# Kernel tuning notes

Hardware: AMD Instinct MI355X
Metric: run time of the kernel (lower is better)

Reference implementation:

```python
import jax, jax.numpy as jnp
import numpy as np
from jax import lax

B, T, D = 16384, 60, 36   # n_traj, n_tp, n_dims
L, C, S = 10, 20, 9       # latent_dim, cluster_num, n_static
OUT = 8                   # mlp out (use_static=False)


def setup_inputs() -> dict:
    key = jax.random.key(0)
    ks = jax.random.split(key, 12)

    def w(k, shape):
        return jax.random.normal(k, shape, jnp.float32) / np.float32(np.sqrt(shape[0]))

    return {
        "data": jax.random.normal(ks[0], (B, T, D), jnp.float32),
        "time_steps": jnp.arange(T, dtype=jnp.float32),
        "static_data": jax.random.normal(ks[1], (B, S), jnp.float32),
        # GRU_unit_cluster gates: Linear(latent_dim + input_dim -> latent_dim)
        "W_update": w(ks[2], (L + D, L)), "b_update": jnp.zeros((L,), jnp.float32),
        "W_reset": w(ks[3], (L + D, L)), "b_reset": jnp.zeros((L,), jnp.float32),
        "W_new": w(ks[4], (L + D, L)), "b_new": jnp.zeros((L,), jnp.float32),
        # infer_emitter_z: Linear(latent_dim + cluster_num -> cluster_num)
        "W_emit": w(ks[5], (L + C, C)), "b_emit": jnp.zeros((C,), jnp.float32),
        # stand-in ODE func (z0_diffeq_solver.ode_func): tanh(Linear(latent->latent))
        "W_ode": w(ks[6], (L, L)), "b_ode": jnp.zeros((L,), jnp.float32),
        # final mlp: Linear(ts*10 + static -> 8)
        "W_mlp": w(ks[7], (T * L + S, OUT)), "b_mlp": jnp.zeros((OUT,), jnp.float32),
    }


def _forward(data, time_steps, static_data,
             W_update, b_update, W_reset, b_reset, W_new, b_new,
             W_emit, b_emit, W_ode, b_ode, W_mlp, b_mlp):
    n_traj = data.shape[0]
    # per-step dt: first step uses the synthetic 0.01 offset, then consecutive diffs
    dts = jnp.concatenate([jnp.full((1,), 0.01, time_steps.dtype), jnp.diff(time_steps)])
    xs = jnp.swapaxes(data, 0, 1)  # [T, B, D]

    def step(carry, inp):
        y_state, y_prob = carry        # [B, L], [B, C]
        x_t, dt = inp                  # [B, D], scalar
        # Euler step of the ODE between observations
        yi_ode = y_state + jnp.tanh(y_state @ W_ode + b_ode) * dt
        # GRU_unit_cluster update
        yc = jnp.concatenate([yi_ode, x_t], axis=-1)          # [B, L+D]
        u = jax.nn.sigmoid(yc @ W_update + b_update)
        r = jax.nn.sigmoid(yc @ W_reset + b_reset)
        cc = jnp.concatenate([yi_ode * r, x_t], axis=-1)
        new = cc @ W_new + b_new
        y_new = (1.0 - u) * new + u * yi_ode                  # [B, L]
        # emit_probs (concat_data=True path)
        zin = jnp.concatenate([y_prob, y_new], axis=-1)       # [B, C+L]
        y_prob_new = jax.nn.softmax(zin @ W_emit + b_emit, axis=-1)
        return (y_new, y_prob_new), y_new

    init = (jnp.zeros((n_traj, L), data.dtype), jnp.zeros((n_traj, C), data.dtype))
    _, states = lax.scan(step, init, (xs, dts))               # states: [T, B, L]

    vec = jnp.swapaxes(states, 0, 1).reshape(n_traj, T * L)   # [B, T*L]
    vec = jnp.concatenate([vec, static_data], axis=-1)        # [B, T*L + S]
    return vec @ W_mlp + b_mlp                                # [B, 8]


def reference(data, time_steps, static_data,
              W_update, b_update, W_reset, b_reset, W_new, b_new,
              W_emit, b_emit, W_ode, b_ode, W_mlp, b_mlp):
    return _forward(data, time_steps, static_data,
                    W_update, b_update, W_reset, b_reset, W_new, b_new,
                    W_emit, b_emit, W_ode, b_ode, W_mlp, b_mlp)
```

## Files before the change

### kernel.cpp

```cpp
#include <hip/hip_runtime.h>
#include <hip/hip_fp16.h>
#include <math.h>

#define B_TRAJ 16384
#define T_STEPS 60
#define D_IN 36
#define L_DIM 10
#define C_NUM 20
#define S_STAT 9
#define OUT_DIM 8
#define TT 2
#define NTILE (T_STEPS / TT)
#define XTS 1824

#define LOG2E 1.4426950408889634f

typedef float f32x2 __attribute__((ext_vector_type(2)));
__device__ __forceinline__ f32x2 pkfma(f32x2 a, f32x2 b, f32x2 c) {
    return __builtin_elementwise_fma(a, b, c);
}

__device__ __forceinline__ float rcp_fast(float x) { return __builtin_amdgcn_rcpf(x); }
__device__ __forceinline__ float exp2_fast(float x) { return __builtin_amdgcn_exp2f(x); }
__device__ __forceinline__ float sigm_fast(float x) {
    return rcp_fast(1.0f + exp2_fast(x * -LOG2E));
}
__device__ __forceinline__ float tanh_fast(float x) {
    const float t = fminf(fmaxf(x * (2.0f * LOG2E), -30.0f), 30.0f);
    return fmaf(-2.0f, rcp_fast(exp2_fast(t) + 1.0f), 1.0f);
}
#define WFENCE() __builtin_amdgcn_wave_barrier()

__global__ __launch_bounds__(256) __attribute__((amdgpu_waves_per_eu(4, 8)))
void dgm2_v8(
    const float* __restrict__ data,
    const float* __restrict__ time_steps,
    const float* __restrict__ static_data,
    const float* __restrict__ W_update,
    const float* __restrict__ b_update,
    const float* __restrict__ W_reset,
    const float* __restrict__ b_reset,
    const float* __restrict__ W_new,
    const float* __restrict__ b_new,
    const float* __restrict__ W_emit,
    const float* __restrict__ b_emit,
    const float* __restrict__ W_ode,
    const float* __restrict__ b_ode,
    const float* __restrict__ W_mlp,
    const float* __restrict__ b_mlp,
    float* __restrict__ out)
{
    __shared__ __align__(16) __half xprojH[8 * XTS];
    __shared__ __align__(16) float wbuf[4][144];
    __shared__ float dts[T_STEPS];

    const int tid  = threadIdx.x;
    const int w    = tid >> 6;
    const int lane = tid & 63;
    const int half = lane >> 5;
    const int s    = lane & 31;
    const int ltraj = w * 2 + half;
    const int traj  = blockIdx.x * 8 + ltraj;
    __half* xpj = xprojH + ltraj * XTS;

    if (tid < T_STEPS) dts[tid] = (tid == 0) ? 0.01f : time_steps[tid] - time_steps[tid - 1];
    __syncthreads();

    const bool uo = (s < 10);
    const bool ro = (s >= 10 && s < 20);
    const bool no = (s >= 20 && s < 30);
    const bool eo = (s >= 10 && s < 30);
    const int  gcol = uo ? s : (ro ? (s - 10) : (no ? (s - 20) : 0));
    const float* Wg = uo ? W_update : (ro ? W_reset : W_new);

    float bcol = 0.0f;
    if (uo)      bcol = b_update[s];
    else if (ro) bcol = b_reset[s - 10];
    else if (no) bcol = b_new[s - 20];

    {
        f32x2 wxp2[18];
#pragma unroll
        for (int j = 0; j < 18; ++j)
            wxp2[j] = (f32x2){Wg[(L_DIM + 2 * j) * L_DIM + gcol],
                              Wg[(L_DIM + 2 * j + 1) * L_DIM + gcol]};

        float* xst = &wbuf[w][0];
        const float* tbase = data + (size_t)(blockIdx.x * 8 + w * 2) * (T_STEPS * D_IN);
        const int sh  = lane / 18;
        const int sr  = lane % 18;
        const int stt = sr / 9;
        const int sc  = sr % 9;
        const bool stg = (lane < 36);

        if (stg) {
            const float4 v = *reinterpret_cast<const float4*>(
                tbase + (size_t)sh * (T_STEPS * D_IN) + stt * D_IN + sc * 4);
            *reinterpret_cast<float4*>(xst + (sh * TT + stt) * 36 + sc * 4) = v;
        }
        WFENCE();

        for (int tile = 0; tile < NTILE; ++tile) {
            float4 pf = make_float4(0.f, 0.f, 0.f, 0.f);
            const bool more = stg && (tile + 1 < NTILE);
            if (more) {
                pf = *reinterpret_cast<const float4*>(
                    tbase + (size_t)sh * (T_STEPS * D_IN) + ((tile + 1) * TT + stt) * D_IN + sc * 4);
            }
#pragma unroll
            for (int tt = 0; tt < TT; ++tt) {
                const float* xrow = xst + (half * TT + tt) * 36;
                f32x2 acc2 = (f32x2){bcol, 0.0f};
#pragma unroll
                for (int c = 0; c < 9; ++c) {
                    const float4 x4 = *reinterpret_cast<const float4*>(xrow + c * 4);
                    acc2 = pkfma((f32x2){x4.x, x4.y}, wxp2[2 * c],     acc2);
                    acc2 = pkfma((f32x2){x4.z, x4.w}, wxp2[2 * c + 1], acc2);
                }
                if (s < 30) xpj[(tile * TT + tt) * 30 + s] = __float2half(acc2.x + acc2.y);
            }
            WFENCE();
            if (more) {
                *reinterpret_cast<float4*>(xst + (sh * TT + stt) * 36 + sc * 4) = pf;
            }
            WFENCE();
        }
    }

    f32x2 wgy2[5];
#pragma unroll
    for (int j = 0; j < 5; ++j)
        wgy2[j] = (f32x2){Wg[(2 * j) * L_DIM + gcol], Wg[(2 * j + 1) * L_DIM + gcol]};

    f32x2 waux2[15];
#pragma unroll
    for (int j = 0; j < 15; ++j) {
        float v0 = 0.0f, v1 = 0.0f;
        if (eo)               { v0 = W_emit[(2 * j) * C_NUM + (s - 10)];
                                v1 = W_emit[(2 * j + 1) * C_NUM + (s - 10)]; }
        else if (uo && j < 5) { v0 = W_ode[(2 * j) * L_DIM + s];
                                v1 = W_ode[(2 * j + 1) * L_DIM + s]; }
        waux2[j] = (f32x2){v0, v1};
    }
    const float bode  = uo ? b_ode[s] : 0.0f;
    const float bemit = eo ? b_emit[s - 10] : 0.0f;

    float* wb   = &wbuf[w][0];
    float* bcYI = wb + 0  + half * 12;
    float* bcR  = wb + 24 + half * 12;
    float* bcU  = wb + 48 + half * 12;
    float* bcY  = wb + 72 + half * 12;
    float* bcP  = wb + 96 + half * 20;

    f32x2 y2[5];
#pragma unroll
    for (int k = 0; k < 5; ++k) y2[k] = (f32x2){0.0f, 0.0f};
    float yown = 0.0f;
    if (eo) bcP[s - 10] = 0.0f;
    WFENCE();

    for (int t = 0; t < T_STEPS; ++t) {
        const float dt = dts[t];

        f32x2 g2 = (f32x2){bode, 0.0f};
#pragma unroll
        for (int k = 0; k < 5; ++k) g2 = pkfma(y2[k], waux2[k], g2);
        const float yis = fmaf(tanh_fast(g2.x + g2.y), dt, yown);
        if (uo) bcYI[s] = yis;
        WFENCE();
        {
            const float4 a = *reinterpret_cast<const float4*>(bcYI);
            const float4 b = *reinterpret_cast<const float4*>(bcYI + 4);
            const float2 c = *reinterpret_cast<const float2*>(bcYI + 8);
            y2[0] = (f32x2){a.x, a.y}; y2[1] = (f32x2){a.z, a.w};
            y2[2] = (f32x2){b.x, b.y}; y2[3] = (f32x2){b.z, b.w};
            y2[4] = (f32x2){c.x, c.y};
        }
        const float yi_g = bcYI[gcol];

        const float xa = __half2float(xpj[t * 30 + s]);
        f32x2 ay2 = (f32x2){xa, 0.0f};
#pragma unroll
        for (int k = 0; k < 5; ++k) ay2 = pkfma(y2[k], wgy2[k], ay2);
        const float uval = sigm_fast(ay2.x + ay2.y);
        if (ro) bcR[s - 10] = uval * yi_g;
        if (uo) bcU[s] = uval;
        WFENCE();

        f32x2 n2 = (f32x2){xa, 0.0f};
        {
            const float4 a = *reinterpret_cast<const float4*>(bcR);
            const float4 b = *reinterpret_cast<const float4*>(bcR + 4);
            const float2 c = *reinterpret_cast<const float2*>(bcR + 8);
            n2 = pkfma((f32x2){a.x, a.y}, wgy2[0], n2);
            n2 = pkfma((f32x2){a.z, a.w}, wgy2[1], n2);
            n2 = pkfma((f32x2){b.x, b.y}, wgy2[2], n2);
            n2 = pkfma((f32x2){b.z, b.w}, wgy2[3], n2);
            n2 = pkfma((f32x2){c.x, c.y}, wgy2[4], n2);
        }
        const float accN = n2.x + n2.y;
        const float u_n  = bcU[gcol];
        const float yn   = fmaf(u_n, yi_g - accN, accN);
        if (no) {
            bcY[s - 20] = yn;
            xpj[t * 30 + (s - 20)] = __float2half(yn);
        }
        WFENCE();
        {
            const float4 a = *reinterpret_cast<const float4*>(bcY);
            const float4 b = *reinterpret_cast<const float4*>(bcY + 4);
            const float2 c = *reinterpret_cast<const float2*>(bcY + 8);
            y2[0] = (f32x2){a.x, a.y}; y2[1] = (f32x2){a.z, a.w};
            y2[2] = (f32x2){b.x, b.y}; y2[3] = (f32x2){b.z, b.w};
            y2[4] = (f32x2){c.x, c.y};
        }
        yown = bcY[gcol];

        f32x2 zd2 = (f32x2){0.0f, 0.0f};
        f32x2 zs2 = (f32x2){0.0f, 0.0f};
#pragma unroll
        for (int q = 0; q < 5; ++q) {
            const float4 z4 = *reinterpret_cast<const float4*>(bcP + q * 4);
            const f32x2 za = (f32x2){z4.x, z4.y};
            const f32x2 zb = (f32x2){z4.z, z4.w};
            zd2 = pkfma(za, waux2[2 * q],     zd2);
            zd2 = pkfma(zb, waux2[2 * q + 1], zd2);
            zs2 = zs2 + za + zb;
        }
        const float zsum = zs2.x + zs2.y;
        const float pinv = (t == 0) ? 0.0f : rcp_fast(zsum);
        f32x2 ev2 = (f32x2){fmaf(zd2.x + zd2.y, pinv, bemit), 0.0f};
#pragma unroll
        for (int k = 0; k < 5; ++k) ev2 = pkfma(y2[k], waux2[10 + k], ev2);
        const float zv = exp2_fast(fminf((ev2.x + ev2.y) * LOG2E, 86.0f));
        if (eo) bcP[s - 10] = zv;
    }

    WFENCE();
    {
        const int g = s >> 3, col = s & 7;
        f32x2 o2 = (f32x2){0.0f, 0.0f};
        for (int tb = 0; tb < 15; ++tb) {
            const int t = g + tb * 4;
            const __half2* yh = reinterpret_cast<const __half2*>(xpj + t * 30);
            const float* wrow = W_mlp + (size_t)t * L_DIM * OUT_DIM + col;
#pragma unroll
            for (int q = 0; q < 5; ++q) {
                const float2 yv = __half22float2(yh[q]);
                const f32x2 w2 = (f32x2){wrow[(2 * q) * OUT_DIM], wrow[(2 * q + 1) * OUT_DIM]};
                o2 = pkfma((f32x2){yv.x, yv.y}, w2, o2);
            }
        }
        float o8 = o2.x + o2.y;
        o8 += __shfl_xor(o8, 8, 32);
        o8 += __shfl_xor(o8, 16, 32);
        if (s < OUT_DIM) {
            const float* stp = static_data + (size_t)traj * S_STAT;
            const float* wms = W_mlp + (size_t)(T_STEPS * L_DIM) * OUT_DIM;
#pragma unroll
            for (int i = 0; i < S_STAT; ++i) o8 += stp[i] * wms[i * OUT_DIM + s];
            out[(size_t)traj * OUT_DIM + s] = o8 + b_mlp[s];
        }
    }
}

extern "C" void kernel_launch(void* const* d_in, const int* in_sizes, int n_in,
                              void* d_out, int out_size, void* d_ws, size_t ws_size,
                              hipStream_t stream) {
    const float* data        = (const float*)d_in[0];
    const float* time_steps  = (const float*)d_in[1];
    const float* static_data = (const float*)d_in[2];
    const float* W_update    = (const float*)d_in[3];
    const float* b_update    = (const float*)d_in[4];
    const float* W_reset     = (const float*)d_in[5];
    const float* b_reset     = (const float*)d_in[6];
    const float* W_new       = (const float*)d_in[7];
    const float* b_new       = (const float*)d_in[8];
    const float* W_emit      = (const float*)d_in[9];
    const float* b_emit      = (const float*)d_in[10];
    const float* W_ode       = (const float*)d_in[11];
    const float* b_ode       = (const float*)d_in[12];
    const float* W_mlp       = (const float*)d_in[13];
    const float* b_mlp       = (const float*)d_in[14];
    float* out = (float*)d_out;

    dim3 grid(B_TRAJ / 8), block(256);
    hipLaunchKernelGGL(dgm2_v8, grid, block, 0, stream,
                       data, time_steps, static_data,
                       W_update, b_update, W_reset, b_reset, W_new, b_new,
                       W_emit, b_emit, W_ode, b_ode, W_mlp, b_mlp, out);
}
```

Measured before the change: 330.6 us.

## Remap recurrence to 16 lanes per trajectory with single-wave blocks

Each trajectory now gets 16 lanes instead of 32. Every lane computes its own update, reset and new gate column, plus up to two emitter columns. The recurrent step drops from four wave-local exchanges to three because the u value no longer needs to be broadcast. Blocks shrink to one wave with four trajectories each, so each wave does twice the useful work and barriers are cheaper. In exchange each lane holds more registers for weights, which may lower occupancy, and the serial dependency chain per lane gets longer.

```diff
diff --git a/kernel.cpp b/kernel.cpp
--- a/kernel.cpp
+++ b/kernel.cpp
@@ -12,6 +12,7 @@
 #define TT 2
 #define NTILE (T_STEPS / TT)
 #define XTS 1824
+#define GSTRIDE 88
 
 #define LOG2E 1.4426950408889634f
 
@@ -19,7 +20,6 @@
 __device__ __forceinline__ f32x2 pkfma(f32x2 a, f32x2 b, f32x2 c) {
     return __builtin_elementwise_fma(a, b, c);
 }
-
 __device__ __forceinline__ float rcp_fast(float x) { return __builtin_amdgcn_rcpf(x); }
 __device__ __forceinline__ float exp2_fast(float x) { return __builtin_amdgcn_exp2f(x); }
 __device__ __forceinline__ float sigm_fast(float x) {
@@ -31,8 +31,8 @@
 }
 #define WFENCE() __builtin_amdgcn_wave_barrier()
 
-__global__ __launch_bounds__(256) __attribute__((amdgpu_waves_per_eu(4, 8)))
-void dgm2_v8(
+__global__ __launch_bounds__(64)
+void dgm2_v9(
     const float* __restrict__ data,
     const float* __restrict__ time_steps,
     const float* __restrict__ static_data,
@@ -50,113 +50,159 @@
     const float* __restrict__ b_mlp,
     float* __restrict__ out)
 {
-    __shared__ __align__(16) __half xprojH[8 * XTS];
-    __shared__ __align__(16) float wbuf[4][144];
+    __shared__ __align__(16) __half xprojH[4 * XTS];
+    __shared__ __align__(16) float wbuf[4 * GSTRIDE];
     __shared__ float dts[T_STEPS];
 
     const int tid  = threadIdx.x;
-    const int w    = tid >> 6;
-    const int lane = tid & 63;
-    const int half = lane >> 5;
-    const int s    = lane & 31;
-    const int ltraj = w * 2 + half;
-    const int traj  = blockIdx.x * 8 + ltraj;
-    __half* xpj = xprojH + ltraj * XTS;
+    const int g    = tid >> 4;
+    const int q    = tid & 15;
+    const int traj = blockIdx.x * 4 + g;
+    __half* xpj = xprojH + g * XTS;
 
     if (tid < T_STEPS) dts[tid] = (tid == 0) ? 0.01f : time_steps[tid] - time_steps[tid - 1];
-    __syncthreads();
-
-    const bool uo = (s < 10);
-    const bool ro = (s >= 10 && s < 20);
-    const bool no = (s >= 20 && s < 30);
-    const bool eo = (s >= 10 && s < 30);
-    const int  gcol = uo ? s : (ro ? (s - 10) : (no ? (s - 20) : 0));
-    const float* Wg = uo ? W_update : (ro ? W_reset : W_new);
-
-    float bcol = 0.0f;
-    if (uo)      bcol = b_update[s];
-    else if (ro) bcol = b_reset[s - 10];
-    else if (no) bcol = b_new[s - 20];
+    WFENCE();
+
+    auto gate_ptr = [&](int c) -> const float* {
+        return c < 10 ? W_update : (c < 20 ? W_reset : W_new);
+    };
+    auto gate_col = [&](int c) -> int { return c < 10 ? c : (c < 20 ? c - 10 : c - 20); };
+    auto gate_bias = [&](int c) -> float {
+        return c < 10 ? b_update[c] : (c < 20 ? b_reset[c - 10] : b_new[c - 20]);
+    };
 
     {
-        f32x2 wxp2[18];
-#pragma unroll
-        for (int j = 0; j < 18; ++j)
-            wxp2[j] = (f32x2){Wg[(L_DIM + 2 * j) * L_DIM + gcol],
-                              Wg[(L_DIM + 2 * j + 1) * L_DIM + gcol]};
-
-        float* xst = &wbuf[w][0];
-        const float* tbase = data + (size_t)(blockIdx.x * 8 + w * 2) * (T_STEPS * D_IN);
-        const int sh  = lane / 18;
-        const int sr  = lane % 18;
-        const int stt = sr / 9;
-        const int sc  = sr % 9;
-        const bool stg = (lane < 36);
-
-        if (stg) {
-            const float4 v = *reinterpret_cast<const float4*>(
-                tbase + (size_t)sh * (T_STEPS * D_IN) + stt * D_IN + sc * 4);
-            *reinterpret_cast<float4*>(xst + (sh * TT + stt) * 36 + sc * 4) = v;
+        const int  c0   = q;
+        const bool has1 = (q < 14);
+        const int  c1   = has1 ? 16 + q : 29;
+        const float* W0 = gate_ptr(c0); const int cc0 = gate_col(c0);
+        const float* W1 = gate_ptr(c1); const int cc1 = gate_col(c1);
+
+        f32x2 wxp0[18], wxp1[18];
+#pragma unroll
+        for (int j = 0; j < 18; ++j) {
+            wxp0[j] = (f32x2){W0[(L_DIM + 2 * j) * L_DIM + cc0],
+                              W0[(L_DIM + 2 * j + 1) * L_DIM + cc0]};
+            const f32x2 v1 = (f32x2){W1[(L_DIM + 2 * j) * L_DIM + cc1],
+                                     W1[(L_DIM + 2 * j + 1) * L_DIM + cc1]};
+            wxp1[j] = has1 ? v1 : (f32x2){0.0f, 0.0f};
+        }
+        const float bcol0 = gate_bias(c0);
+        const float bcol1 = has1 ? gate_bias(c1) : 0.0f;
+
+        float* stagef = wbuf;
+        const float* tb0 = data + (size_t)(blockIdx.x * 4) * (T_STEPS * D_IN);
+        const int a_tr = tid / 18, a_rm = tid % 18, a_tt = a_rm / 9, a_c = a_rm % 9;
+        const int bch = 64 + tid;
+        const int b_tr = bch / 18, b_rm = bch % 18, b_tt = b_rm / 9, b_c = b_rm % 9;
+        const bool hb = (tid < 8);
+
+        {
+            const float4 v0 = *reinterpret_cast<const float4*>(
+                tb0 + (size_t)a_tr * (T_STEPS * D_IN) + a_tt * D_IN + a_c * 4);
+            *reinterpret_cast<float4*>(stagef + (a_tr * TT + a_tt) * 36 + a_c * 4) = v0;
+            if (hb) {
+                const float4 v1 = *reinterpret_cast<const float4*>(
+                    tb0 + (size_t)b_tr * (T_STEPS * D_IN) + b_tt * D_IN + b_c * 4);
+                *reinterpret_cast<float4*>(stagef + (b_tr * TT + b_tt) * 36 + b_c * 4) = v1;
+            }
         }
         WFENCE();
 
         for (int tile = 0; tile < NTILE; ++tile) {
-            float4 pf = make_float4(0.f, 0.f, 0.f, 0.f);
-            const bool more = stg && (tile + 1 < NTILE);
+            float4 pf0 = {}, pf1 = {};
+            const bool more = (tile + 1 < NTILE);
             if (more) {
-                pf = *reinterpret_cast<const float4*>(
-                    tbase + (size_t)sh * (T_STEPS * D_IN) + ((tile + 1) * TT + stt) * D_IN + sc * 4);
+                pf0 = *reinterpret_cast<const float4*>(
+                    tb0 + (size_t)a_tr * (T_STEPS * D_IN) + ((tile + 1) * TT + a_tt) * D_IN + a_c * 4);
+                if (hb)
+                    pf1 = *reinterpret_cast<const float4*>(
+                        tb0 + (size_t)b_tr * (T_STEPS * D_IN) + ((tile + 1) * TT + b_tt) * D_IN + b_c * 4);
             }
 #pragma unroll
             for (int tt = 0; tt < TT; ++tt) {
-                const float* xrow = xst + (half * TT + tt) * 36;
-                f32x2 acc2 = (f32x2){bcol, 0.0f};
+                const float* xrow = stagef + (g * TT + tt) * 36;
+                f32x2 acc0 = (f32x2){bcol0, 0.0f};
+                f32x2 acc1 = (f32x2){bcol1, 0.0f};
 #pragma unroll
                 for (int c = 0; c < 9; ++c) {
                     const float4 x4 = *reinterpret_cast<const float4*>(xrow + c * 4);
-                    acc2 = pkfma((f32x2){x4.x, x4.y}, wxp2[2 * c],     acc2);
-                    acc2 = pkfma((f32x2){x4.z, x4.w}, wxp2[2 * c + 1], acc2);
+                    const f32x2 xlo = (f32x2){x4.x, x4.y};
+                    const f32x2 xhi = (f32x2){x4.z, x4.w};
+                    acc0 = pkfma(xlo, wxp0[2 * c], acc0);
+                    acc0 = pkfma(xhi, wxp0[2 * c + 1], acc0);
+                    acc1 = pkfma(xlo, wxp1[2 * c], acc1);
+                    acc1 = pkfma(xhi, wxp1[2 * c + 1], acc1);
                 }
-                if (s < 30) xpj[(tile * TT + tt) * 30 + s] = __float2half(acc2.x + acc2.y);
+                const int row = (tile * TT + tt) * 30;
+                xpj[row + q] = __float2half(acc0.x + acc0.y);
+                if (has1) xpj[row + 16 + q] = __float2half(acc1.x + acc1.y);
             }
             WFENCE();
             if (more) {
-                *reinterpret_cast<float4*>(xst + (sh * TT + stt) * 36 + sc * 4) = pf;
+                *reinterpret_cast<float4*>(stagef + (a_tr * TT + a_tt) * 36 + a_c * 4) = pf0;
+                if (hb)
+                    *reinterpret_cast<float4*>(stagef + (b_tr * TT + b_tt) * 36 + b_c * 4) = pf1;
             }
             WFENCE();
         }
     }
 
-    f32x2 wgy2[5];
-#pragma unroll
-    for (int j = 0; j < 5; ++j)
-        wgy2[j] = (f32x2){Wg[(2 * j) * L_DIM + gcol], Wg[(2 * j + 1) * L_DIM + gcol]};
-
-    f32x2 waux2[15];
-#pragma unroll
-    for (int j = 0; j < 15; ++j) {
-        float v0 = 0.0f, v1 = 0.0f;
-        if (eo)               { v0 = W_emit[(2 * j) * C_NUM + (s - 10)];
-                                v1 = W_emit[(2 * j + 1) * C_NUM + (s - 10)]; }
-        else if (uo && j < 5) { v0 = W_ode[(2 * j) * L_DIM + s];
-                                v1 = W_ode[(2 * j + 1) * L_DIM + s]; }
-        waux2[j] = (f32x2){v0, v1};
-    }
-    const float bode  = uo ? b_ode[s] : 0.0f;
-    const float bemit = eo ? b_emit[s - 10] : 0.0f;
-
-    float* wb   = &wbuf[w][0];
-    float* bcYI = wb + 0  + half * 12;
-    float* bcR  = wb + 24 + half * 12;
-    float* bcU  = wb + 48 + half * 12;
-    float* bcY  = wb + 72 + half * 12;
-    float* bcP  = wb + 96 + half * 20;
+    const bool qg = (q < 10);
+    f32x2 wode2[5], wu2[5], wr2[5], wn2[5];
+#pragma unroll
+    for (int j = 0; j < 5; ++j) {
+        if (qg) {
+            wode2[j] = (f32x2){W_ode[(2 * j) * L_DIM + q], W_ode[(2 * j + 1) * L_DIM + q]};
+            wu2[j]   = (f32x2){W_update[(2 * j) * L_DIM + q], W_update[(2 * j + 1) * L_DIM + q]};
+            wr2[j]   = (f32x2){W_reset[(2 * j) * L_DIM + q], W_reset[(2 * j + 1) * L_DIM + q]};
+            wn2[j]   = (f32x2){W_new[(2 * j) * L_DIM + q], W_new[(2 * j + 1) * L_DIM + q]};
+        } else {
+            wode2[j] = wu2[j] = wr2[j] = wn2[j] = (f32x2){0.0f, 0.0f};
+        }
+    }
+    const float bode = qg ? b_ode[q] : 0.0f;
+
+    const int  e0  = q;
+    const bool he1 = (q < 4);
+    const int  e1  = he1 ? 16 + q : 19;
+    f32x2 wez0[10], wez1[10], wey0[5], wey1[5];
+#pragma unroll
+    for (int j = 0; j < 10; ++j) {
+        wez0[j] = (f32x2){W_emit[(2 * j) * C_NUM + e0], W_emit[(2 * j + 1) * C_NUM + e0]};
+        const f32x2 v1 = (f32x2){W_emit[(2 * j) * C_NUM + e1], W_emit[(2 * j + 1) * C_NUM + e1]};
+        wez1[j] = he1 ? v1 : (f32x2){0.0f, 0.0f};
+    }
+#pragma unroll
+    for (int j = 0; j < 5; ++j) {
+        wey0[j] = (f32x2){W_emit[(C_NUM + 2 * j) * C_NUM + e0], W_emit[(C_NUM + 2 * j + 1) * C_NUM + e0]};
+        const f32x2 v1 = (f32x2){W_emit[(C_NUM + 2 * j) * C_NUM + e1], W_emit[(C_NUM + 2 * j + 1) * C_NUM + e1]};
+        wey1[j] = he1 ? v1 : (f32x2){0.0f, 0.0f};
+    }
+    const float be0 = b_emit[e0];
+    const float be1 = he1 ? b_emit[e1] : 0.0f;
+
+    float* grp = wbuf + g * GSTRIDE;
+    float* gYI = grp;
+    float* gYR = grp + 16;
+    float* gY  = grp + 32;
+    float* gZ  = grp + 48;
+
+    auto ldvec = [&](const float* p, f32x2* d) {
+        const float4 a = *reinterpret_cast<const float4*>(p);
+        const float4 b = *reinterpret_cast<const float4*>(p + 4);
+        const float2 c = *reinterpret_cast<const float2*>(p + 8);
+        d[0] = (f32x2){a.x, a.y}; d[1] = (f32x2){a.z, a.w};
+        d[2] = (f32x2){b.x, b.y}; d[3] = (f32x2){b.z, b.w};
+        d[4] = (f32x2){c.x, c.y};
+    };
 
     f32x2 y2[5];
 #pragma unroll
     for (int k = 0; k < 5; ++k) y2[k] = (f32x2){0.0f, 0.0f};
     float yown = 0.0f;
-    if (eo) bcP[s - 10] = 0.0f;
+    gZ[q] = 0.0f;
+    if (he1) gZ[16 + q] = 0.0f;
     WFENCE();
 
     for (int t = 0; t < T_STEPS; ++t) {
@@ -164,102 +210,100 @@
 
         f32x2 g2 = (f32x2){bode, 0.0f};
 #pragma unroll
-        for (int k = 0; k < 5; ++k) g2 = pkfma(y2[k], waux2[k], g2);
+        for (int k = 0; k < 5; ++k) g2 = pkfma(y2[k], wode2[k], g2);
         const float yis = fmaf(tanh_fast(g2.x + g2.y), dt, yown);
-        if (uo) bcYI[s] = yis;
+        gYI[q] = yis;
         WFENCE();
+        f32x2 yi2[5];
+        ldvec(gYI, yi2);
+
+        const float xau = __half2float(xpj[t * 30 + q]);
+        const float xar = __half2float(xpj[t * 30 + 10 + q]);
+        const float xan = __half2float(xpj[t * 30 + 20 + q]);
+        f32x2 au2 = (f32x2){xau, 0.0f};
+        f32x2 ar2 = (f32x2){xar, 0.0f};
+#pragma unroll
+        for (int k = 0; k < 5; ++k) {
+            au2 = pkfma(yi2[k], wu2[k], au2);
+            ar2 = pkfma(yi2[k], wr2[k], ar2);
+        }
+        const float u = sigm_fast(au2.x + au2.y);
+        const float r = sigm_fast(ar2.x + ar2.y);
+        gYR[q] = r * yis;
+        WFENCE();
+        f32x2 yr2[5];
+        ldvec(gYR, yr2);
+
+        f32x2 an2 = (f32x2){xan, 0.0f};
+#pragma unroll
+        for (int k = 0; k < 5; ++k) an2 = pkfma(yr2[k], wn2[k], an2);
+        const float nv = an2.x + an2.y;
+        const float yn = fmaf(u, yis - nv, nv);
+        yown = yn;
+        gY[q] = yn;
+        xpj[t * 30 + q] = __float2half(yn);
+        WFENCE();
+        ldvec(gY, y2);
+
+        f32x2 zz[10];
         {
-            const float4 a = *reinterpret_cast<const float4*>(bcYI);
-            const float4 b = *reinterpret_cast<const float4*>(bcYI + 4);
-            const float2 c = *reinterpret_cast<const float2*>(bcYI + 8);
-            y2[0] = (f32x2){a.x, a.y}; y2[1] = (f32x2){a.z, a.w};
-            y2[2] = (f32x2){b.x, b.y}; y2[3] = (f32x2){b.z, b.w};
-            y2[4] = (f32x2){c.x, c.y};
-        }
-        const float yi_g = bcYI[gcol];
-
-        const float xa = __half2float(xpj[t * 30 + s]);
-        f32x2 ay2 = (f32x2){xa, 0.0f};
-#pragma unroll
-        for (int k = 0; k < 5; ++k) ay2 = pkfma(y2[k], wgy2[k], ay2);
-        const float uval = sigm_fast(ay2.x + ay2.y);
-        if (ro) bcR[s - 10] = uval * yi_g;
-        if (uo) bcU[s] = uval;
-        WFENCE();
-
-        f32x2 n2 = (f32x2){xa, 0.0f};
-        {
-            const float4 a = *reinterpret_cast<const float4*>(bcR);
-            const float4 b = *reinterpret_cast<const float4*>(bcR + 4);
-            const float2 c = *reinterpret_cast<const float2*>(bcR + 8);
-            n2 = pkfma((f32x2){a.x, a.y}, wgy2[0], n2);
-            n2 = pkfma((f32x2){a.z, a.w}, wgy2[1], n2);
-            n2 = pkfma((f32x2){b.x, b.y}, wgy2[2], n2);
-            n2 = pkfma((f32x2){b.z, b.w}, wgy2[3], n2);
-            n2 = pkfma((f32x2){c.x, c.y}, wgy2[4], n2);
-        }
-        const float accN = n2.x + n2.y;
-        const float u_n  = bcU[gcol];
-        const float yn   = fmaf(u_n, yi_g - accN, accN);
-        if (no) {
-            bcY[s - 20] = yn;
-            xpj[t * 30 + (s - 20)] = __float2half(yn);
-        }
-        WFENCE();
-        {
-            const float4 a = *reinterpret_cast<const float4*>(bcY);
-            const float4 b = *reinterpret_cast<const float4*>(bcY + 4);
-            const float2 c = *reinterpret_cast<const float2*>(bcY + 8);
-            y2[0] = (f32x2){a.x, a.y}; y2[1] = (f32x2){a.z, a.w};
-            y2[2] = (f32x2){b.x, b.y}; y2[3] = (f32x2){b.z, b.w};
-            y2[4] = (f32x2){c.x, c.y};
-        }
-        yown = bcY[gcol];
-
-        f32x2 zd2 = (f32x2){0.0f, 0.0f};
+            const float4 z0 = *reinterpret_cast<const float4*>(gZ);
+            const float4 z1 = *reinterpret_cast<const float4*>(gZ + 4);
+            const float4 z2 = *reinterpret_cast<const float4*>(gZ + 8);
+            const float4 z3 = *reinterpret_cast<const float4*>(gZ + 12);
+            const float4 z4 = *reinterpret_cast<const float4*>(gZ + 16);
+            zz[0] = (f32x2){z0.x, z0.y}; zz[1] = (f32x2){z0.z, z0.w};
+            zz[2] = (f32x2){z1.x, z1.y}; zz[3] = (f32x2){z1.z, z1.w};
+            zz[4] = (f32x2){z2.x, z2.y}; zz[5] = (f32x2){z2.z, z2.w};
+            zz[6] = (f32x2){z3.x, z3.y}; zz[7] = (f32x2){z3.z, z3.w};
+            zz[8] = (f32x2){z4.x, z4.y}; zz[9] = (f32x2){z4.z, z4.w};
+        }
+        f32x2 zd0 = (f32x2){0.0f, 0.0f}, zd1 = (f32x2){0.0f, 0.0f};
         f32x2 zs2 = (f32x2){0.0f, 0.0f};
 #pragma unroll
-        for (int q = 0; q < 5; ++q) {
-            const float4 z4 = *reinterpret_cast<const float4*>(bcP + q * 4);
-            const f32x2 za = (f32x2){z4.x, z4.y};
-            const f32x2 zb = (f32x2){z4.z, z4.w};
-            zd2 = pkfma(za, waux2[2 * q],     zd2);
-            zd2 = pkfma(zb, waux2[2 * q + 1], zd2);
-            zs2 = zs2 + za + zb;
+        for (int j = 0; j < 10; ++j) {
+            zd0 = pkfma(zz[j], wez0[j], zd0);
+            zd1 = pkfma(zz[j], wez1[j], zd1);
+            zs2 = zs2 + zz[j];
         }
         const float zsum = zs2.x + zs2.y;
         const float pinv = (t == 0) ? 0.0f : rcp_fast(zsum);
-        f32x2 ev2 = (f32x2){fmaf(zd2.x + zd2.y, pinv, bemit), 0.0f};
-#pragma unroll
-        for (int k = 0; k < 5; ++k) ev2 = pkfma(y2[k], waux2[10 + k], ev2);
-        const float zv = exp2_fast(fminf((ev2.x + ev2.y) * LOG2E, 86.0f));
-        if (eo) bcP[s - 10] = zv;
+        f32x2 ev0 = (f32x2){fmaf(zd0.x + zd0.y, pinv, be0), 0.0f};
+        f32x2 ev1 = (f32x2){fmaf(zd1.x + zd1.y, pinv, be1), 0.0f};
+#pragma unroll
+        for (int k = 0; k < 5; ++k) {
+            ev0 = pkfma(y2[k], wey0[k], ev0);
+            ev1 = pkfma(y2[k], wey1[k], ev1);
+        }
+        const float zv0 = exp2_fast(fminf((ev0.x + ev0.y) * LOG2E, 86.0f));
+        const float zv1 = exp2_fast(fminf((ev1.x + ev1.y) * LOG2E, 86.0f));
+        gZ[q] = zv0;
+        if (he1) gZ[16 + q] = zv1;
     }
 
     WFENCE();
     {
-        const int g = s >> 3, col = s & 7;
+        const int col = q & 7, tg = q >> 3;
         f32x2 o2 = (f32x2){0.0f, 0.0f};
-        for (int tb = 0; tb < 15; ++tb) {
-            const int t = g + tb * 4;
+        for (int tb = 0; tb < 30; ++tb) {
+            const int t = tb * 2 + tg;
             const __half2* yh = reinterpret_cast<const __half2*>(xpj + t * 30);
             const float* wrow = W_mlp + (size_t)t * L_DIM * OUT_DIM + col;
 #pragma unroll
-            for (int q = 0; q < 5; ++q) {
-                const float2 yv = __half22float2(yh[q]);
-                const f32x2 w2 = (f32x2){wrow[(2 * q) * OUT_DIM], wrow[(2 * q + 1) * OUT_DIM]};
+            for (int q4 = 0; q4 < 5; ++q4) {
+                const float2 yv = __half22float2(yh[q4]);
+                const f32x2 w2 = (f32x2){wrow[(2 * q4) * OUT_DIM], wrow[(2 * q4 + 1) * OUT_DIM]};
                 o2 = pkfma((f32x2){yv.x, yv.y}, w2, o2);
             }
         }
         float o8 = o2.x + o2.y;
-        o8 += __shfl_xor(o8, 8, 32);
-        o8 += __shfl_xor(o8, 16, 32);
-        if (s < OUT_DIM) {
+        o8 += __shfl_xor(o8, 8, 16);
+        if (q < OUT_DIM) {
             const float* stp = static_data + (size_t)traj * S_STAT;
             const float* wms = W_mlp + (size_t)(T_STEPS * L_DIM) * OUT_DIM;
 #pragma unroll
-            for (int i = 0; i < S_STAT; ++i) o8 += stp[i] * wms[i * OUT_DIM + s];
-            out[(size_t)traj * OUT_DIM + s] = o8 + b_mlp[s];
+            for (int i = 0; i < S_STAT; ++i) o8 += stp[i] * wms[i * OUT_DIM + q];
+            out[(size_t)traj * OUT_DIM + q] = o8 + b_mlp[q];
         }
     }
 }
@@ -284,8 +328,8 @@
     const float* b_mlp       = (const float*)d_in[14];
     float* out = (float*)d_out;
 
-    dim3 grid(B_TRAJ / 8), block(256);
-    hipLaunchKernelGGL(dgm2_v8, grid, block, 0, stream,
+    dim3 grid(B_TRAJ / 4), block(64);
+    hipLaunchKernelGGL(dgm2_v9, grid, block, 0, stream,
                        data, time_steps, static_data,
                        W_update, b_update, W_reset, b_reset, W_new, b_new,
                        W_emit, b_emit, W_ode, b_ode, W_mlp, b_mlp, out);
```

Result: no change. 332.3 us (+0.5%).

## Chunk input projection into two halves and fuse MLP head into recurrence

Applied to the files above, without the earlier changes.

Splits the precomputed half-precision input projection into two 30-step chunks, so each trajectory needs half the LDS buffer, and halves the block to 128 threads with a higher waves-per-EU hint. The final MLP head is now accumulated step by step inside the recurrence instead of storing states and doing a separate pass afterwards. This cuts LDS footprint to raise occupancy. In exchange it pays for a mid-sequence refill that reloads the projection weights and stalls the serial recurrence, and adds global W_mlp loads on every step.

```diff
diff --git a/kernel.cpp b/kernel.cpp
--- a/kernel.cpp
+++ b/kernel.cpp
@@ -10,8 +10,10 @@
 #define S_STAT 9
 #define OUT_DIM 8
 #define TT 2
-#define NTILE (T_STEPS / TT)
-#define XTS 1824
+#define CHT 30
+#define NTILE_C (CHT / TT)
+#define XTS2 928
+#define WBF 184
 
 #define LOG2E 1.4426950408889634f
 
@@ -19,7 +21,6 @@
 __device__ __forceinline__ f32x2 pkfma(f32x2 a, f32x2 b, f32x2 c) {
     return __builtin_elementwise_fma(a, b, c);
 }
-
 __device__ __forceinline__ float rcp_fast(float x) { return __builtin_amdgcn_rcpf(x); }
 __device__ __forceinline__ float exp2_fast(float x) { return __builtin_amdgcn_exp2f(x); }
 __device__ __forceinline__ float sigm_fast(float x) {
@@ -31,8 +32,8 @@
 }
 #define WFENCE() __builtin_amdgcn_wave_barrier()
 
-__global__ __launch_bounds__(256) __attribute__((amdgpu_waves_per_eu(4, 8)))
-void dgm2_v8(
+__global__ __launch_bounds__(128) __attribute__((amdgpu_waves_per_eu(6, 8)))
+void dgm2_v14(
     const float* __restrict__ data,
     const float* __restrict__ time_steps,
     const float* __restrict__ static_data,
@@ -50,8 +51,8 @@
     const float* __restrict__ b_mlp,
     float* __restrict__ out)
 {
-    __shared__ __align__(16) __half xprojH[8 * XTS];
-    __shared__ __align__(16) float wbuf[4][144];
+    __shared__ __align__(16) __half xprojH[4 * XTS2];
+    __shared__ __align__(16) float wbuf[2][WBF];
     __shared__ float dts[T_STEPS];
 
     const int tid  = threadIdx.x;
@@ -60,8 +61,8 @@
     const int half = lane >> 5;
     const int s    = lane & 31;
     const int ltraj = w * 2 + half;
-    const int traj  = blockIdx.x * 8 + ltraj;
-    __half* xpj = xprojH + ltraj * XTS;
+    const int traj  = blockIdx.x * 4 + ltraj;
+    __half* xpj = xprojH + ltraj * XTS2;
 
     if (tid < T_STEPS) dts[tid] = (tid == 0) ? 0.01f : time_steps[tid] - time_steps[tid - 1];
     __syncthreads();
@@ -72,60 +73,6 @@
     const bool eo = (s >= 10 && s < 30);
     const int  gcol = uo ? s : (ro ? (s - 10) : (no ? (s - 20) : 0));
     const float* Wg = uo ? W_update : (ro ? W_reset : W_new);
-
-    float bcol = 0.0f;
-    if (uo)      bcol = b_update[s];
-    else if (ro) bcol = b_reset[s - 10];
-    else if (no) bcol = b_new[s - 20];
-
-    {
-        f32x2 wxp2[18];
-#pragma unroll
-        for (int j = 0; j < 18; ++j)
-            wxp2[j] = (f32x2){Wg[(L_DIM + 2 * j) * L_DIM + gcol],
-                              Wg[(L_DIM + 2 * j + 1) * L_DIM + gcol]};
-
-        float* xst = &wbuf[w][0];
-        const float* tbase = data + (size_t)(blockIdx.x * 8 + w * 2) * (T_STEPS * D_IN);
-        const int sh  = lane / 18;
-        const int sr  = lane % 18;
-        const int stt = sr / 9;
-        const int sc  = sr % 9;
-        const bool stg = (lane < 36);
-
-        if (stg) {
-            const float4 v = *reinterpret_cast<const float4*>(
-                tbase + (size_t)sh * (T_STEPS * D_IN) + stt * D_IN + sc * 4);
-            *reinterpret_cast<float4*>(xst + (sh * TT + stt) * 36 + sc * 4) = v;
-        }
-        WFENCE();
-
-        for (int tile = 0; tile < NTILE; ++tile) {
-            float4 pf = make_float4(0.f, 0.f, 0.f, 0.f);
-            const bool more = stg && (tile + 1 < NTILE);
-            if (more) {
-                pf = *reinterpret_cast<const float4*>(
-                    tbase + (size_t)sh * (T_STEPS * D_IN) + ((tile + 1) * TT + stt) * D_IN + sc * 4);
-            }
-#pragma unroll
-            for (int tt = 0; tt < TT; ++tt) {
-                const float* xrow = xst + (half * TT + tt) * 36;
-                f32x2 acc2 = (f32x2){bcol, 0.0f};
-#pragma unroll
-                for (int c = 0; c < 9; ++c) {
-                    const float4 x4 = *reinterpret_cast<const float4*>(xrow + c * 4);
-                    acc2 = pkfma((f32x2){x4.x, x4.y}, wxp2[2 * c],     acc2);
-                    acc2 = pkfma((f32x2){x4.z, x4.w}, wxp2[2 * c + 1], acc2);
-                }
-                if (s < 30) xpj[(tile * TT + tt) * 30 + s] = __float2half(acc2.x + acc2.y);
-            }
-            WFENCE();
-            if (more) {
-                *reinterpret_cast<float4*>(xst + (sh * TT + stt) * 36 + sc * 4) = pf;
-            }
-            WFENCE();
-        }
-    }
 
     f32x2 wgy2[5];
 #pragma unroll
@@ -145,12 +92,86 @@
     const float bode  = uo ? b_ode[s] : 0.0f;
     const float bemit = eo ? b_emit[s - 10] : 0.0f;
 
+    const int hcol = s & 7;
+    const int kq   = s >> 3;
+    const int boff = 2 * kq * OUT_DIM + hcol;
+    const int hoff = 2 * kq;
+    float phead = 0.0f;
+
     float* wb   = &wbuf[w][0];
-    float* bcYI = wb + 0  + half * 12;
-    float* bcR  = wb + 24 + half * 12;
-    float* bcU  = wb + 48 + half * 12;
-    float* bcY  = wb + 72 + half * 12;
-    float* bcP  = wb + 96 + half * 20;
+    float* bcYI = wb + 0   + half * 12;
+    float* bcR  = wb + 24  + half * 12;
+    float* bcU  = wb + 48  + half * 12;
+    float* bcY  = wb + 72  + half * 12;
+    float* bcP  = wb + 144 + half * 20;
+
+    auto ldvec = [&](const float* p, f32x2* d) {
+        const float4 a = *reinterpret_cast<const float4*>(p);
+        const float4 b = *reinterpret_cast<const float4*>(p + 4);
+        const float2 c = *reinterpret_cast<const float2*>(p + 8);
+        d[0] = (f32x2){a.x, a.y}; d[1] = (f32x2){a.z, a.w};
+        d[2] = (f32x2){b.x, b.y}; d[3] = (f32x2){b.z, b.w};
+        d[4] = (f32x2){c.x, c.y};
+    };
+
+    auto refill = [&](int c) {
+        asm volatile("" ::: "memory");
+        int off = 0;
+        asm volatile("" : "+v"(off));
+        f32x2 wxp2[18];
+#pragma unroll
+        for (int j = 0; j < 18; ++j)
+            wxp2[j] = (f32x2){Wg[(L_DIM + 2 * j) * L_DIM + gcol + off],
+                              Wg[(L_DIM + 2 * j + 1) * L_DIM + gcol + off]};
+        float bcol = 0.0f;
+        if (uo)      bcol = b_update[s];
+        else if (ro) bcol = b_reset[s - 10];
+        else if (no) bcol = b_new[s - 20];
+
+        float* xst = wb;
+        const float* tbase = data + (size_t)(blockIdx.x * 4 + w * 2) * (T_STEPS * D_IN);
+        const int sh  = lane / 18;
+        const int sr  = lane % 18;
+        const int stt = sr / 9;
+        const int scq = sr % 9;
+        const bool stg = (lane < 36);
+        const int cbase = c * CHT;
+
+        if (stg) {
+            const float4 v = *reinterpret_cast<const float4*>(
+                tbase + (size_t)sh * (T_STEPS * D_IN) + (cbase + stt) * D_IN + scq * 4);
+            *reinterpret_cast<float4*>(xst + (sh * TT + stt) * 36 + scq * 4) = v;
+        }
+        WFENCE();
+
+#pragma unroll 1
+        for (int tile = 0; tile < NTILE_C; ++tile) {
+            float4 pf = make_float4(0.f, 0.f, 0.f, 0.f);
+            const bool more = stg && (tile + 1 < NTILE_C);
+            if (more) {
+                pf = *reinterpret_cast<const float4*>(
+                    tbase + (size_t)sh * (T_STEPS * D_IN)
+                          + (cbase + (tile + 1) * TT + stt) * D_IN + scq * 4);
+            }
+#pragma unroll
+            for (int tt = 0; tt < TT; ++tt) {
+                const float* xrow = xst + (half * TT + tt) * 36;
+                f32x2 acc2 = (f32x2){bcol, 0.0f};
+#pragma unroll
+                for (int cq = 0; cq < 9; ++cq) {
+                    const float4 x4 = *reinterpret_cast<const float4*>(xrow + cq * 4);
+                    acc2 = pkfma((f32x2){x4.x, x4.y}, wxp2[2 * cq],     acc2);
+                    acc2 = pkfma((f32x2){x4.z, x4.w}, wxp2[2 * cq + 1], acc2);
+                }
+                if (s < 30) xpj[(tile * TT + tt) * 30 + s] = __float2half(acc2.x + acc2.y);
+            }
+            WFENCE();
+            if (more) {
+                *reinterpret_cast<float4*>(xst + (sh * TT + stt) * 36 + scq * 4) = pf;
+            }
+            WFENCE();
+        }
+    };
 
     f32x2 y2[5];
 #pragma unroll
@@ -159,108 +180,94 @@
     if (eo) bcP[s - 10] = 0.0f;
     WFENCE();
 
-    for (int t = 0; t < T_STEPS; ++t) {
-        const float dt = dts[t];
-
-        f32x2 g2 = (f32x2){bode, 0.0f};
-#pragma unroll
-        for (int k = 0; k < 5; ++k) g2 = pkfma(y2[k], waux2[k], g2);
-        const float yis = fmaf(tanh_fast(g2.x + g2.y), dt, yown);
-        if (uo) bcYI[s] = yis;
-        WFENCE();
-        {
-            const float4 a = *reinterpret_cast<const float4*>(bcYI);
-            const float4 b = *reinterpret_cast<const float4*>(bcYI + 4);
-            const float2 c = *reinterpret_cast<const float2*>(bcYI + 8);
-            y2[0] = (f32x2){a.x, a.y}; y2[1] = (f32x2){a.z, a.w};
-            y2[2] = (f32x2){b.x, b.y}; y2[3] = (f32x2){b.z, b.w};
-            y2[4] = (f32x2){c.x, c.y};
-        }
-        const float yi_g = bcYI[gcol];
-
-        const float xa = __half2float(xpj[t * 30 + s]);
-        f32x2 ay2 = (f32x2){xa, 0.0f};
-#pragma unroll
-        for (int k = 0; k < 5; ++k) ay2 = pkfma(y2[k], wgy2[k], ay2);
-        const float uval = sigm_fast(ay2.x + ay2.y);
-        if (ro) bcR[s - 10] = uval * yi_g;
-        if (uo) bcU[s] = uval;
-        WFENCE();
-
-        f32x2 n2 = (f32x2){xa, 0.0f};
-        {
-            const float4 a = *reinterpret_cast<const float4*>(bcR);
-            const float4 b = *reinterpret_cast<const float4*>(bcR + 4);
-            const float2 c = *reinterpret_cast<const float2*>(bcR + 8);
-            n2 = pkfma((f32x2){a.x, a.y}, wgy2[0], n2);
-            n2 = pkfma((f32x2){a.z, a.w}, wgy2[1], n2);
-            n2 = pkfma((f32x2){b.x, b.y}, wgy2[2], n2);
-            n2 = pkfma((f32x2){b.z, b.w}, wgy2[3], n2);
-            n2 = pkfma((f32x2){c.x, c.y}, wgy2[4], n2);
-        }
-        const float accN = n2.x + n2.y;
-        const float u_n  = bcU[gcol];
-        const float yn   = fmaf(u_n, yi_g - accN, accN);
-        if (no) {
-            bcY[s - 20] = yn;
-            xpj[t * 30 + (s - 20)] = __float2half(yn);
-        }
-        WFENCE();
-        {
-            const float4 a = *reinterpret_cast<const float4*>(bcY);
-            const float4 b = *reinterpret_cast<const float4*>(bcY + 4);
-            const float2 c = *reinterpret_cast<const float2*>(bcY + 8);
-            y2[0] = (f32x2){a.x, a.y}; y2[1] = (f32x2){a.z, a.w};
-            y2[2] = (f32x2){b.x, b.y}; y2[3] = (f32x2){b.z, b.w};
-            y2[4] = (f32x2){c.x, c.y};
-        }
-        yown = bcY[gcol];
-
-        f32x2 zd2 = (f32x2){0.0f, 0.0f};
-        f32x2 zs2 = (f32x2){0.0f, 0.0f};
-#pragma unroll
-        for (int q = 0; q < 5; ++q) {
-            const float4 z4 = *reinterpret_cast<const float4*>(bcP + q * 4);
-            const f32x2 za = (f32x2){z4.x, z4.y};
-            const f32x2 zb = (f32x2){z4.z, z4.w};
-            zd2 = pkfma(za, waux2[2 * q],     zd2);
-            zd2 = pkfma(zb, waux2[2 * q + 1], zd2);
-            zs2 = zs2 + za + zb;
-        }
-        const float zsum = zs2.x + zs2.y;
-        const float pinv = (t == 0) ? 0.0f : rcp_fast(zsum);
-        f32x2 ev2 = (f32x2){fmaf(zd2.x + zd2.y, pinv, bemit), 0.0f};
-#pragma unroll
-        for (int k = 0; k < 5; ++k) ev2 = pkfma(y2[k], waux2[10 + k], ev2);
-        const float zv = exp2_fast(fminf((ev2.x + ev2.y) * LOG2E, 86.0f));
-        if (eo) bcP[s - 10] = zv;
+    refill(0);
+    WFENCE();
+
+#pragma unroll 1
+    for (int c = 0; c < 2; ++c) {
+#pragma unroll 1
+        for (int tt = 0; tt < CHT; ++tt) {
+            const int t = c * CHT + tt;
+            const float dt = dts[t];
+
+            f32x2 g2 = (f32x2){bode, 0.0f};
+#pragma unroll
+            for (int k = 0; k < 5; ++k) g2 = pkfma(y2[k], waux2[k], g2);
+            const float yis = fmaf(tanh_fast(g2.x + g2.y), dt, yown);
+            if (uo) bcYI[s] = yis;
+            WFENCE();
+            f32x2 yi2[5];
+            ldvec(bcYI, yi2);
+            const float yi_g = bcYI[gcol];
+
+            const float xa = __half2float(xpj[tt * 30 + s]);
+            f32x2 ay2 = (f32x2){xa, 0.0f};
+#pragma unroll
+            for (int k = 0; k < 5; ++k) ay2 = pkfma(yi2[k], wgy2[k], ay2);
+            const float uval = sigm_fast(ay2.x + ay2.y);
+            if (ro) bcR[s - 10] = uval * yi_g;
+            if (uo) bcU[s] = uval;
+            WFENCE();
+            f32x2 yr2[5];
+            ldvec(bcR, yr2);
+
+            f32x2 n2 = (f32x2){xa, 0.0f};
+#pragma unroll
+            for (int k = 0; k < 5; ++k) n2 = pkfma(yr2[k], wgy2[k], n2);
+            const float accN = n2.x + n2.y;
+            const float u_n  = bcU[gcol];
+            const float yn   = fmaf(u_n, yi_g - accN, accN);
+            if (no) bcY[s - 20] = yn;
+            WFENCE();
+            ldvec(bcY, y2);
+            yown = bcY[gcol];
+
+            {
+                const float* wr = W_mlp + (size_t)t * (L_DIM * OUT_DIM);
+                const f32x2 yh = *reinterpret_cast<const f32x2*>(bcY + hoff);
+                phead = fmaf(yh.x, wr[boff], phead);
+                phead = fmaf(yh.y, wr[boff + OUT_DIM], phead);
+                if (kq == 0) {
+                    phead = fmaf(y2[4].x, wr[8 * OUT_DIM + hcol], phead);
+                    phead = fmaf(y2[4].y, wr[9 * OUT_DIM + hcol], phead);
+                }
+            }
+
+            f32x2 zz[10];
+#pragma unroll
+            for (int j = 0; j < 5; ++j) {
+                const float4 z = *reinterpret_cast<const float4*>(bcP + j * 4);
+                zz[2 * j] = (f32x2){z.x, z.y}; zz[2 * j + 1] = (f32x2){z.z, z.w};
+            }
+            f32x2 zd2 = (f32x2){0.0f, 0.0f};
+            f32x2 zs2 = (f32x2){0.0f, 0.0f};
+#pragma unroll
+            for (int j = 0; j < 10; ++j) {
+                zd2 = pkfma(zz[j], waux2[j], zd2);
+                zs2 = zs2 + zz[j];
+            }
+            const float pinv = (t == 0) ? 0.0f : rcp_fast(zs2.x + zs2.y);
+            f32x2 ev2 = (f32x2){fmaf(zd2.x + zd2.y, pinv, bemit), 0.0f};
+#pragma unroll
+            for (int k = 0; k < 5; ++k) ev2 = pkfma(y2[k], waux2[10 + k], ev2);
+            const float zv = exp2_fast(fminf((ev2.x + ev2.y) * LOG2E, 86.0f));
+            if (eo) bcP[s - 10] = zv;
+        }
+        if (c == 0) {
+            refill(1);
+            WFENCE();
+        }
     }
 
-    WFENCE();
-    {
-        const int g = s >> 3, col = s & 7;
-        f32x2 o2 = (f32x2){0.0f, 0.0f};
-        for (int tb = 0; tb < 15; ++tb) {
-            const int t = g + tb * 4;
-            const __half2* yh = reinterpret_cast<const __half2*>(xpj + t * 30);
-            const float* wrow = W_mlp + (size_t)t * L_DIM * OUT_DIM + col;
-#pragma unroll
-            for (int q = 0; q < 5; ++q) {
-                const float2 yv = __half22float2(yh[q]);
-                const f32x2 w2 = (f32x2){wrow[(2 * q) * OUT_DIM], wrow[(2 * q + 1) * OUT_DIM]};
-                o2 = pkfma((f32x2){yv.x, yv.y}, w2, o2);
-            }
-        }
-        float o8 = o2.x + o2.y;
-        o8 += __shfl_xor(o8, 8, 32);
-        o8 += __shfl_xor(o8, 16, 32);
-        if (s < OUT_DIM) {
-            const float* stp = static_data + (size_t)traj * S_STAT;
-            const float* wms = W_mlp + (size_t)(T_STEPS * L_DIM) * OUT_DIM;
-#pragma unroll
-            for (int i = 0; i < S_STAT; ++i) o8 += stp[i] * wms[i * OUT_DIM + s];
-            out[(size_t)traj * OUT_DIM + s] = o8 + b_mlp[s];
-        }
+    phead += __shfl_xor(phead, 8, 32);
+    phead += __shfl_xor(phead, 16, 32);
+    if (s < OUT_DIM) {
+        const float* stp = static_data + (size_t)traj * S_STAT;
+        const float* wms = W_mlp + (size_t)(T_STEPS * L_DIM) * OUT_DIM;
+        float o = phead;
+#pragma unroll
+        for (int i = 0; i < S_STAT; ++i) o += stp[i] * wms[i * OUT_DIM + s];
+        out[(size_t)traj * OUT_DIM + s] = o + b_mlp[s];
     }
 }
 
@@ -284,8 +291,8 @@
     const float* b_mlp       = (const float*)d_in[14];
     float* out = (float*)d_out;
 
-    dim3 grid(B_TRAJ / 8), block(256);
-    hipLaunchKernelGGL(dgm2_v8, grid, block, 0, stream,
+    dim3 grid(B_TRAJ / 4), block(128);
+    hipLaunchKernelGGL(dgm2_v14, grid, block, 0, stream,
                        data, time_steps, static_data,
                        W_update, b_update, W_reset, b_reset, W_new, b_new,
                        W_emit, b_emit, W_ode, b_ode, W_mlp, b_mlp, out);
```

New measurement: 1.297 ms. 292% more time.
